# Optimization experiments

Measured on AMD Instinct MI355X. Metric: run time of the kernel, lower is better.

The kernel has to match this reference:

```python
import jax, jax.numpy as jnp
import numpy as np

SIGMA = 10.0   # init kwarg sigma
NODE_IDX = 28  # teeth per arch
P = 320        # points per tooth
D = 3


def setup_inputs() -> dict:
    key = jax.random.key(0)
    k1, k2 = jax.random.split(key)
    X_v = jax.random.normal(k1, (NODE_IDX, P, D), dtype=jnp.float32)
    target_X_v = jax.random.normal(k2, (NODE_IDX, P, D), dtype=jnp.float32)
    return {"X_v": X_v, "target_X_v": target_X_v, "node_idx": NODE_IDX}


def _chamfer_sum(x, y):
    # x: [N,3], y: [M,3]. Squared-L2 chamfer with point_reduction='sum' both
    # directions and batch_reduction='sum' (batch size 1) as in pytorch3d.
    d = (jnp.sum(x * x, axis=-1)[:, None]
         + jnp.sum(y * y, axis=-1)[None, :]
         - 2.0 * (x @ y.T))  # [N, M] squared distances
    return jnp.min(d, axis=1).sum() + jnp.min(d, axis=0).sum()


def _gather_idx(node_idx):
    # Per-node subset: drop node idx, append paired node (idx+mid or idx-mid).
    mid = (node_idx - 2) // 2
    rows = []
    for idx in range(node_idx - 2):
        extra = idx + mid if idx < mid else idx - mid
        rows.append([j for j in range(node_idx) if j != idx] + [extra])
    return np.asarray(rows, dtype=np.int32), mid


def reference(X_v, target_X_v, node_idx):
    n, p, d = X_v.shape
    cX = jnp.clip(X_v, -SIGMA, SIGMA)
    cT = jnp.clip(target_X_v, -SIGMA, SIGMA)
    idx_mat, mid = _gather_idx(node_idx)           # [node_idx-2, node_idx]
    subs_x = cX[idx_mat].reshape(node_idx - 2, n * p, d)
    subs_t = cT[idx_mat].reshape(node_idx - 2, n * p, d)

    def body(acc, xt):
        x, t = xt
        return acc + _chamfer_sum(x, t), None

    loss, _ = jax.lax.scan(body, jnp.float32(0.0), (subs_x, subs_t))
    # idx == node_idx-2: first half of the arch; idx == node_idx-1: second half
    loss = loss + _chamfer_sum(cX[:mid].reshape(-1, d), cT[:mid].reshape(-1, d))
    loss = loss + _chamfer_sum(cX[mid:].reshape(-1, d), cT[mid:].reshape(-1, d))
    return loss
```

## Files before the change

### kernel.cpp

```cpp
#include <hip/hip_runtime.h>

#define NODES  28
#define PPN    320
#define MID    13
#define NPTS   (NODES * PPN)
#define TOTPTS (2 * NPTS)
#define SIGMA  10.0f
#define FLT_BIG 3.4e38f

#define BT    128
#define RPT   2
#define GPTS  (BT * RPT)
#define NGRP  (NPTS / GPTS)

__device__ float g_m[NODES][TOTPTS];

__global__ __launch_bounds__(BT)
void pair_min_kernel(const float* __restrict__ X, const float* __restrict__ T,
                     float* __restrict__ out)
{
    __shared__ float4 st[PPN];

    const int bid = blockIdx.x;
    const int p   = bid / (NGRP * NODES);
    const int r   = bid % (NGRP * NODES);
    const int g   = r / NODES;
    const int b   = r % NODES;

    const float* __restrict__ src = p ? T : X;
    const float* __restrict__ db  = p ? X : T;

    const int t = threadIdx.x;

    if (bid == 0 && t == 0) *out = 0.0f;

    for (int j = t; j < PPN; j += BT) {
        const float* q = db + (size_t)(b * PPN + j) * 3;
        float v0 = fminf(fmaxf(q[0], -SIGMA), SIGMA);
        float v1 = fminf(fmaxf(q[1], -SIGMA), SIGMA);
        float v2 = fminf(fmaxf(q[2], -SIGMA), SIGMA);
        float n  = v0*v0 + v1*v1 + v2*v2;
        st[j] = make_float4(-2.f*v0, -2.f*v1, -2.f*v2, n);
    }

    const int i0 = g * GPTS + t;
    const int i1 = i0 + BT;
    float4 s0, s1;
    {
        const float* q0 = src + (size_t)i0 * 3;
        float a0 = fminf(fmaxf(q0[0], -SIGMA), SIGMA);
        float a1 = fminf(fmaxf(q0[1], -SIGMA), SIGMA);
        float a2 = fminf(fmaxf(q0[2], -SIGMA), SIGMA);
        s0 = make_float4(a0, a1, a2, a0*a0 + a1*a1 + a2*a2);
        const float* q1 = src + (size_t)i1 * 3;
        float b0 = fminf(fmaxf(q1[0], -SIGMA), SIGMA);
        float b1 = fminf(fmaxf(q1[1], -SIGMA), SIGMA);
        float b2 = fminf(fmaxf(q1[2], -SIGMA), SIGMA);
        s1 = make_float4(b0, b1, b2, b0*b0 + b1*b1 + b2*b2);
    }
    __syncthreads();

    float mn0 = FLT_BIG, mn1 = FLT_BIG;
    #pragma unroll 4
    for (int j = 0; j < PPN; j += 2) {
        const float4 ta = st[j];
        const float4 tb = st[j + 1];
        float d0a = fmaf(ta.x, s0.x, fmaf(ta.y, s0.y, fmaf(ta.z, s0.z, ta.w)));
        float d0b = fmaf(tb.x, s0.x, fmaf(tb.y, s0.y, fmaf(tb.z, s0.z, tb.w)));
        float d1a = fmaf(ta.x, s1.x, fmaf(ta.y, s1.y, fmaf(ta.z, s1.z, ta.w)));
        float d1b = fmaf(tb.x, s1.x, fmaf(tb.y, s1.y, fmaf(tb.z, s1.z, tb.w)));
        mn0 = fminf(mn0, fminf(d0a, d0b));
        mn1 = fminf(mn1, fminf(d1a, d1b));
    }

    const int q0 = p * NPTS + i0;
    g_m[b][q0]      = mn0 + s0.w;
    g_m[b][q0 + BT] = mn1 + s1.w;
}

__inline__ __device__ float wave_reduce_sum(float v) {
    #pragma unroll
    for (int off = 32; off > 0; off >>= 1)
        v += __shfl_down(v, off, 64);
    return v;
}

__global__ __launch_bounds__(256)
void combine_kernel(float* __restrict__ out)
{
    const int q = blockIdx.x * blockDim.x + threadIdx.x;
    float tot = 0.0f;
    if (q < TOTPTS) {
        const int a = (q % NPTS) / PPN;

        float r[NODES];
        #pragma unroll
        for (int c = 0; c < NODES; ++c) r[c] = g_m[c][q];

        float min1 = FLT_BIG; int c1 = -1;
        #pragma unroll
        for (int c = 0; c < NODES; ++c) {
            if (r[c] < min1) { min1 = r[c]; c1 = c; }
        }
        float min2 = FLT_BIG;
        #pragma unroll
        for (int c = 0; c < NODES; ++c) {
            float v = (c == c1) ? FLT_BIG : r[c];
            min2 = fminf(min2, v);
        }
        float H = FLT_BIG;
        if (a < MID) {
            #pragma unroll
            for (int c = 0; c < MID; ++c) H = fminf(H, r[c]);
        } else {
            #pragma unroll
            for (int c = MID; c < NODES; ++c) H = fminf(H, r[c]);
        }

        const int n = (a < NODES - 2) ? (NODES - 3) : (NODES - 2);
        float S = (float)n * min1;
        if (c1 <= NODES - 3 && c1 != a) S -= (min1 - min2);
        if (a < NODES - 2) {
            const int dup = (a < MID) ? (a + MID) : (a - MID);
            S += (c1 == dup) ? min2 : min1;
        }
        tot = S + H;
    }

    __shared__ float warp_sums[4];
    float ws = wave_reduce_sum(tot);
    const int lane = threadIdx.x & 63;
    const int wid  = threadIdx.x >> 6;
    if (lane == 0) warp_sums[wid] = ws;
    __syncthreads();
    if (wid == 0) {
        float v = (lane < 4) ? warp_sums[lane] : 0.0f;
        v = wave_reduce_sum(v);
        if (lane == 0) atomicAdd(out, v);
    }
}

extern "C" void kernel_launch(void* const* d_in, const int* in_sizes, int n_in,
                              void* d_out, int out_size, void* d_ws, size_t ws_size,
                              hipStream_t stream) {
    const float* X = (const float*)d_in[0];
    const float* T = (const float*)d_in[1];
    float* out = (float*)d_out;
    (void)d_ws; (void)ws_size;

    pair_min_kernel<<<2 * NGRP * NODES, BT, 0, stream>>>(X, T, out);
    combine_kernel<<<(TOTPTS + 255) / 256, 256, 0, stream>>>(out);
}
```

Before: 74.78 us.

## Fuse pair-min and combine kernels with last-arriver tail reduction

Merges the two launches into one kernel. Each block atomically counts arrivals per point group, and the last of the 28 node blocks for that group does the combine step over those points. A global tail counter then lets the final group sum the per-group partials deterministically into the output. This removes a kernel launch and the inter-kernel gap, at the cost of fences, atomics, and a serial tail done by a few blocks.

Result: slower. 198.1 us (+164.9%).

```diff
diff --git a/kernel.cpp b/kernel.cpp
--- a/kernel.cpp
+++ b/kernel.cpp
@@ -8,31 +8,44 @@
 #define SIGMA  10.0f
 #define FLT_BIG 3.4e38f
 
-#define BT    128
-#define RPT   2
-#define GPTS  (BT * RPT)
-#define NGRP  (NPTS / GPTS)
+#define BT      128
+#define RPT     2
+#define GPTS    (BT * RPT)
+#define NGRP    (NPTS / GPTS)
+#define NGROUPS (2 * NGRP)
+#define NBLK    (NGROUPS * NODES)
 
 __device__ float g_m[NODES][TOTPTS];
+__device__ float g_part[NGROUPS];
+__device__ unsigned int g_arrive[NGROUPS];
+__device__ unsigned int g_tailcnt;
+
+__inline__ __device__ float wave_reduce_sum(float v) {
+    #pragma unroll
+    for (int off = 32; off > 0; off >>= 1)
+        v += __shfl_down(v, off, 64);
+    return v;
+}
 
 __global__ __launch_bounds__(BT)
-void pair_min_kernel(const float* __restrict__ X, const float* __restrict__ T,
-                     float* __restrict__ out)
+void chamfer_fused(const float* __restrict__ X, const float* __restrict__ T,
+                   float* __restrict__ out)
 {
     __shared__ float4 st[PPN];
+    __shared__ float  redf[2];
+    __shared__ int    s_tail;
 
     const int bid = blockIdx.x;
     const int p   = bid / (NGRP * NODES);
     const int r   = bid % (NGRP * NODES);
     const int g   = r / NODES;
     const int b   = r % NODES;
+    const int pg  = p * NGRP + g;
 
     const float* __restrict__ src = p ? T : X;
     const float* __restrict__ db  = p ? X : T;
 
     const int t = threadIdx.x;
-
-    if (bid == 0 && t == 0) *out = 0.0f;
 
     for (int j = t; j < PPN; j += BT) {
         const float* q = db + (size_t)(b * PPN + j) * 3;
@@ -47,15 +60,15 @@
     const int i1 = i0 + BT;
     float4 s0, s1;
     {
-        const float* q0 = src + (size_t)i0 * 3;
-        float a0 = fminf(fmaxf(q0[0], -SIGMA), SIGMA);
-        float a1 = fminf(fmaxf(q0[1], -SIGMA), SIGMA);
-        float a2 = fminf(fmaxf(q0[2], -SIGMA), SIGMA);
+        const float* q0p = src + (size_t)i0 * 3;
+        float a0 = fminf(fmaxf(q0p[0], -SIGMA), SIGMA);
+        float a1 = fminf(fmaxf(q0p[1], -SIGMA), SIGMA);
+        float a2 = fminf(fmaxf(q0p[2], -SIGMA), SIGMA);
         s0 = make_float4(a0, a1, a2, a0*a0 + a1*a1 + a2*a2);
-        const float* q1 = src + (size_t)i1 * 3;
-        float b0 = fminf(fmaxf(q1[0], -SIGMA), SIGMA);
-        float b1 = fminf(fmaxf(q1[1], -SIGMA), SIGMA);
-        float b2 = fminf(fmaxf(q1[2], -SIGMA), SIGMA);
+        const float* q1p = src + (size_t)i1 * 3;
+        float b0 = fminf(fmaxf(q1p[0], -SIGMA), SIGMA);
+        float b1 = fminf(fmaxf(q1p[1], -SIGMA), SIGMA);
+        float b2 = fminf(fmaxf(q1p[2], -SIGMA), SIGMA);
         s1 = make_float4(b0, b1, b2, b0*b0 + b1*b1 + b2*b2);
     }
     __syncthreads();
@@ -76,45 +89,47 @@
     const int q0 = p * NPTS + i0;
     g_m[b][q0]      = mn0 + s0.w;
     g_m[b][q0 + BT] = mn1 + s1.w;
-}
 
-__inline__ __device__ float wave_reduce_sum(float v) {
+    __threadfence();
+    __syncthreads();
+    if (t == 0) {
+        unsigned int old = atomicAdd(&g_arrive[pg], 1u);
+        s_tail = ((old % NODES) == NODES - 1) ? 1 : 0;
+    }
+    __syncthreads();
+    if (!s_tail) return;
+
+    __threadfence();
+
+    float tot = 0.0f;
     #pragma unroll
-    for (int off = 32; off > 0; off >>= 1)
-        v += __shfl_down(v, off, 64);
-    return v;
-}
+    for (int k = 0; k < RPT; ++k) {
+        const int ql = g * GPTS + t + k * BT;
+        const int q  = p * NPTS + ql;
+        const int a  = ql / PPN;
 
-__global__ __launch_bounds__(256)
-void combine_kernel(float* __restrict__ out)
-{
-    const int q = blockIdx.x * blockDim.x + threadIdx.x;
-    float tot = 0.0f;
-    if (q < TOTPTS) {
-        const int a = (q % NPTS) / PPN;
-
-        float r[NODES];
+        float rr[NODES];
         #pragma unroll
-        for (int c = 0; c < NODES; ++c) r[c] = g_m[c][q];
+        for (int c = 0; c < NODES; ++c) rr[c] = g_m[c][q];
 
         float min1 = FLT_BIG; int c1 = -1;
         #pragma unroll
         for (int c = 0; c < NODES; ++c) {
-            if (r[c] < min1) { min1 = r[c]; c1 = c; }
+            if (rr[c] < min1) { min1 = rr[c]; c1 = c; }
         }
         float min2 = FLT_BIG;
         #pragma unroll
         for (int c = 0; c < NODES; ++c) {
-            float v = (c == c1) ? FLT_BIG : r[c];
+            float v = (c == c1) ? FLT_BIG : rr[c];
             min2 = fminf(min2, v);
         }
         float H = FLT_BIG;
         if (a < MID) {
             #pragma unroll
-            for (int c = 0; c < MID; ++c) H = fminf(H, r[c]);
+            for (int c = 0; c < MID; ++c) H = fminf(H, rr[c]);
         } else {
             #pragma unroll
-            for (int c = MID; c < NODES; ++c) H = fminf(H, r[c]);
+            for (int c = MID; c < NODES; ++c) H = fminf(H, rr[c]);
         }
 
         const int n = (a < NODES - 2) ? (NODES - 3) : (NODES - 2);
@@ -124,19 +139,26 @@
             const int dup = (a < MID) ? (a + MID) : (a - MID);
             S += (c1 == dup) ? min2 : min1;
         }
-        tot = S + H;
+        tot += S + H;
     }
 
-    __shared__ float warp_sums[4];
     float ws = wave_reduce_sum(tot);
-    const int lane = threadIdx.x & 63;
-    const int wid  = threadIdx.x >> 6;
-    if (lane == 0) warp_sums[wid] = ws;
+    const int lane = t & 63;
+    const int wid  = t >> 6;
+    if (lane == 0) redf[wid] = ws;
     __syncthreads();
-    if (wid == 0) {
-        float v = (lane < 4) ? warp_sums[lane] : 0.0f;
-        v = wave_reduce_sum(v);
-        if (lane == 0) atomicAdd(out, v);
+    if (t == 0) {
+        float bs = redf[0] + redf[1];
+        atomicExch(&g_part[pg], bs);
+        __threadfence();
+        unsigned int old = atomicAdd(&g_tailcnt, 1u);
+        if ((old % NGROUPS) == NGROUPS - 1) {
+            __threadfence();
+            float s = 0.0f;
+            for (int i = 0; i < NGROUPS; ++i)
+                s += atomicAdd(&g_part[i], 0.0f);
+            *out = s;
+        }
     }
 }
 
@@ -148,6 +170,5 @@
     float* out = (float*)d_out;
     (void)d_ws; (void)ws_size;
 
-    pair_min_kernel<<<2 * NGRP * NODES, BT, 0, stream>>>(X, T, out);
-    combine_kernel<<<(TOTPTS + 255) / 256, 256, 0, stream>>>(out);
+    chamfer_fused<<<NBLK, BT, 0, stream>>>(X, T, out);
 }
```
